# Performance work log

Measured on AMD Instinct MI355X. Metric: run time of the kernel, lower is better.

## Reference

```python
import jax, jax.numpy as jnp
import numpy as np

B, T, K = 1024, 1024, 48
START, STOP = 46, 47
NEG = -10000.0


def setup_inputs() -> dict:
    key = jax.random.key(0)
    k1, k2 = jax.random.split(key)
    feats = jax.random.normal(k1, (B, T, K), dtype=jnp.float32)
    transitions = jax.random.normal(k2, (K, K), dtype=jnp.float32)
    # CRF constraints exactly as in __init__: no transition into START, none out of STOP
    transitions = transitions.at[START, :].set(NEG).at[:, STOP].set(NEG)
    return {"feats": feats, "transitions": transitions}


def _viterbi_one(feats, transitions):
    # feats: [T, K]; transitions[next_tag, prev_tag]: [K, K]
    init = jnp.full((K,), NEG, dtype=feats.dtype).at[START].set(0.0)

    def step(forward_var, feat):
        # scores[next, prev] = forward_var[prev] + transitions[next, prev]
        scores = forward_var[None, :] + transitions
        bptr = jnp.argmax(scores, axis=1)                 # [K] best prev per next
        new_fv = jnp.max(scores, axis=1) + feat           # [K]
        return new_fv, bptr

    forward_var, bptrs = jax.lax.scan(step, init, feats)  # bptrs: [T, K]
    terminal = forward_var + transitions[STOP]
    best = jnp.argmax(terminal)
    path_score = terminal[best]

    # backtrack: carry = tag at time t, emit it, move to bptrs[t][tag]
    def back(tag, bp):
        return bp[tag], tag

    _, best_path = jax.lax.scan(back, best, bptrs, reverse=True)  # [T] in time order
    return path_score, best_path


def reference(feats, transitions):
    # vmap the (faithful, per-sequence) Viterbi decode over the batch
    scores, paths = jax.vmap(_viterbi_one, in_axes=(0, None))(feats, transitions)
    return scores, paths
```

## Files before the change

kernel.cpp:

```cpp
#include <hip/hip_runtime.h>
#include <float.h>


#define BB 1024
#define TT 1024
#define KK 48
#define CC 16
#define LL 64
#define NEGV -10000.0f

__device__ __forceinline__ float rdlane(float v, int l) {
  return __int_as_float(__builtin_amdgcn_readlane(__float_as_int(v), l));
}
__device__ __forceinline__ float max3f(float a, float b, float c) {
  return fmaxf(fmaxf(a, b), c);
}


#define FSTEP(T_, FEAT_)                                                   \
  {                                                                        \
    float fvs[KK];                                                         \
    _Pragma("unroll") for (int p = 0; p < KK; ++p) {                       \
      fvs[p] = rdlane(fv, p);                                              \
    }                                                                      \
    float s_[KK];                                                          \
    _Pragma("unroll") for (int p = 0; p < KK; ++p) {                       \
      s_[p] = fvs[p] + tr[p];                                              \
    }                                                                      \
    float part[16];                                                        \
    _Pragma("unroll") for (int g = 0; g < 16; ++g) {                       \
      part[g] = max3f(s_[3 * g], s_[3 * g + 1], s_[3 * g + 2]);            \
    }                                                                      \
    float q0 = max3f(part[0], part[1], part[2]);                           \
    float q1 = max3f(part[3], part[4], part[5]);                           \
    float q2 = max3f(part[6], part[7], part[8]);                           \
    float q3 = max3f(part[9], part[10], part[11]);                         \
    float q4 = max3f(part[12], part[13], part[14]);                        \
    float m_ = fmaxf(max3f(q0, q1, q2), max3f(q3, q4, part[15]));          \
    mp[(size_t)(T_)*KK] = m_;                                              \
    fv = m_ + (FEAT_);                                                     \
  }

__global__ __launch_bounds__(64, 1) void viterbi_fwd_mx(
    const float* __restrict__ feats, const float* __restrict__ trans,
    float* __restrict__ scores, float* __restrict__ mx,
    int* __restrict__ bestArr) {
  const int lane = threadIdx.x;
  const int b = blockIdx.x;
  const int rl = (lane < KK) ? lane : (KK - 1);

  float tr[KK];
#pragma unroll
  for (int j = 0; j < 12; ++j) {
    float4 t4 = *(const float4*)(trans + rl * KK + 4 * j);
    tr[4 * j + 0] = t4.x; tr[4 * j + 1] = t4.y;
    tr[4 * j + 2] = t4.z; tr[4 * j + 3] = t4.w;
  }
#pragma unroll
  for (int j = 0; j < KK; ++j) asm volatile("" : "+v"(tr[j]));
  const float tstop = trans[(KK - 1) * KK + rl];

  const float* fp = feats + (size_t)b * TT * KK + rl;
  float* mp = mx + (size_t)b * TT * KK + rl;

  float fv = (lane == 46) ? 0.0f : NEGV;

  float fA[8], fB[8];
#pragma unroll
  for (int k = 0; k < 8; ++k) fA[k] = fp[(size_t)k * KK];

  for (int t0 = 0; t0 < TT; t0 += 16) {
#pragma unroll
    for (int k = 0; k < 8; ++k)
      fB[k] = fp[(size_t)((t0 + 8 + k) & (TT - 1)) * KK];
#pragma unroll
    for (int u = 0; u < 8; ++u) FSTEP(t0 + u, fA[u]);
#pragma unroll
    for (int k = 0; k < 8; ++k)
      fA[k] = fp[(size_t)((t0 + 16 + k) & (TT - 1)) * KK];
#pragma unroll
    for (int u = 0; u < 8; ++u) FSTEP(t0 + 8 + u, fB[u]);
  }

  float v = (lane < KK) ? (fv + tstop) : -FLT_MAX;
  int idx = lane;
#pragma unroll
  for (int off = 32; off >= 1; off >>= 1) {
    float ov = __shfl_xor(v, off);
    int oi = __shfl_xor(idx, off);
    bool take = (ov > v) || (ov == v && oi < idx);
    v = take ? ov : v;
    idx = take ? oi : idx;
  }
  if (lane == 0) { scores[b] = v; bestArr[b] = idx; }
}

__global__ __launch_bounds__(64, 1) void viterbi_bwd_mx(
    const float* __restrict__ feats, const float* __restrict__ trans,
    const float* __restrict__ mx, const int* __restrict__ bestArr,
    float* __restrict__ path) {
  __shared__ float tl[KK * KK];
  const int lane = threadIdx.x;
  const int b = blockIdx.x;
  const int rl = (lane < KK) ? lane : (KK - 1);
  for (int i = lane; i < KK * KK; i += 64) tl[i] = trans[i];
  __syncthreads();

  const float* fp = feats + (size_t)b * TT * KK + rl;
  const float* mp = mx + (size_t)b * TT * KK + rl;
  int tag = bestArr[b];

  float topA = mp[(size_t)(TT - 1) * KK];
  float MA[8], FE[8], MB[8], FB2[8];
#pragma unroll
  for (int u = 0; u < 8; ++u) {
    MA[u] = mp[(size_t)(TT - 2 - u) * KK];
    FE[u] = fp[(size_t)(TT - 2 - u) * KK];
  }

  int myv = 0;
  for (int jb = TT - 1; jb >= 15; jb -= 16) {
#pragma unroll
    for (int u = 0; u < 8; ++u) {
      int r = jb - 9 - u; int rc = r < 0 ? 0 : r;
      MB[u] = mp[(size_t)rc * KK];
      FB2[u] = fp[(size_t)rc * KK];
    }
#pragma unroll
    for (int u = 0; u < 8; ++u) {
      const int j = jb - u;
      if (lane == (j & 63)) myv = tag;
      if ((j & 63) == 0) path[(size_t)b * TT + j + lane] = (float)myv;
      float Tg = (u == 0) ? topA : MA[u - 1];
      float target = rdlane(Tg, tag);
      float s = (MA[u] + FE[u]) + tl[tag * KK + rl];
      unsigned long long bal = __ballot(s == target);
      tag = (int)__builtin_ctzll(bal);
    }
    float topB = MA[7];
#pragma unroll
    for (int u = 0; u < 8; ++u) {
      int r = jb - 17 - u; int rc = r < 0 ? 0 : r;
      MA[u] = mp[(size_t)rc * KK];
      FE[u] = fp[(size_t)rc * KK];
    }
#pragma unroll
    for (int u = 0; u < 8; ++u) {
      const int j = jb - 8 - u;
      if (lane == (j & 63)) myv = tag;
      if ((j & 63) == 0) path[(size_t)b * TT + j + lane] = (float)myv;
      float Tg = (u == 0) ? topB : MB[u - 1];
      float target = rdlane(Tg, tag);
      float s = (MB[u] + FB2[u]) + tl[tag * KK + rl];
      unsigned long long bal = __ballot(s == target);
      tag = (int)__builtin_ctzll(bal);
    }
    topA = MB[7];
  }
}


__global__ __launch_bounds__(64, 1) void viterbi_fwd_f(
    const float* __restrict__ feats, const float* __restrict__ trans,
    float* __restrict__ scores, unsigned char* __restrict__ bptr,
    int* __restrict__ bestArr) {
  __shared__ __align__(16) float fvbuf[64];
  const int lane = threadIdx.x;
  const int b = blockIdx.x;
  const int rl = (lane < KK) ? lane : (KK - 1);

  float tr[KK];
#pragma unroll
  for (int j = 0; j < 12; ++j) {
    float4 t4 = *(const float4*)(trans + rl * KK + 4 * j);
    tr[4 * j + 0] = t4.x; tr[4 * j + 1] = t4.y;
    tr[4 * j + 2] = t4.z; tr[4 * j + 3] = t4.w;
  }
  const float tstop = trans[(KK - 1) * KK + rl];

  if (lane < KK) fvbuf[lane] = (lane == 46) ? 0.0f : NEGV;
  __builtin_amdgcn_wave_barrier();

  const float* fp = feats + (size_t)b * TT * KK + rl;
  unsigned char* bp = bptr + (size_t)b * TT * KK + lane;

  float fbuf[4];
#pragma unroll
  for (int k = 0; k < 4; ++k) fbuf[k] = fp[(size_t)k * KK];

  float fv = NEGV;
  for (int t0 = 0; t0 < TT; t0 += 4) {
#pragma unroll
    for (int u = 0; u < 4; ++u) {
      const int t = t0 + u;
      float fvr[KK];
#pragma unroll
      for (int j = 0; j < 12; ++j) {
        float4 v4 = *(const float4*)(&fvbuf[4 * j]);
        fvr[4 * j + 0] = v4.x; fvr[4 * j + 1] = v4.y;
        fvr[4 * j + 2] = v4.z; fvr[4 * j + 3] = v4.w;
      }
      __builtin_amdgcn_wave_barrier();

      float bs0 = fvr[0] + tr[0], bs1 = fvr[12] + tr[12];
      float bs2 = fvr[24] + tr[24], bs3 = fvr[36] + tr[36];
      int bi0 = 0, bi1 = 12, bi2 = 24, bi3 = 36;
#pragma unroll
      for (int p = 1; p < 12; ++p) {
        float s0 = fvr[p] + tr[p];
        float s1 = fvr[12 + p] + tr[12 + p];
        float s2 = fvr[24 + p] + tr[24 + p];
        float s3 = fvr[36 + p] + tr[36 + p];
        if (s0 > bs0) { bs0 = s0; bi0 = p; }
        if (s1 > bs1) { bs1 = s1; bi1 = 12 + p; }
        if (s2 > bs2) { bs2 = s2; bi2 = 24 + p; }
        if (s3 > bs3) { bs3 = s3; bi3 = 36 + p; }
      }
      bool c1 = bs1 > bs0;
      float m01 = c1 ? bs1 : bs0; int i01 = c1 ? bi1 : bi0;
      bool c3 = bs3 > bs2;
      float m23 = c3 ? bs3 : bs2; int i23 = c3 ? bi3 : bi2;
      bool cf = m23 > m01;
      float m = cf ? m23 : m01; int bpi = cf ? i23 : i01;

      float nfv = m + fbuf[u];
      int tpre = t + 4; if (tpre >= TT) tpre = 0;
      fbuf[u] = fp[(size_t)tpre * KK];

      if (lane < KK) {
        bp[(size_t)t * KK] = (unsigned char)bpi;
        fvbuf[lane] = nfv;
        fv = nfv;
      }
      __builtin_amdgcn_wave_barrier();
    }
  }

  float v = (lane < KK) ? (fv + tstop) : -FLT_MAX;
  int idx = lane;
#pragma unroll
  for (int off = 32; off >= 1; off >>= 1) {
    float ov = __shfl_xor(v, off);
    int oi = __shfl_xor(idx, off);
    bool take = (ov > v) || (ov == v && oi < idx);
    v = take ? ov : v;
    idx = take ? oi : idx;
  }
  if (lane == 0) { scores[b] = v; bestArr[b] = idx; }
}

__global__ __launch_bounds__(256) void bwd_map(
    const unsigned char* __restrict__ bptr, unsigned char* __restrict__ cmap) {
  const int lane = threadIdx.x & 63;
  const int wg = blockIdx.x * 4 + (threadIdx.x >> 6);
  const int b = wg >> 4;
  const int c = wg & (CC - 1);
  const int rl = (lane < KK) ? lane : (KK - 1);
  const unsigned char* bp = bptr + ((size_t)b * TT + (size_t)c * LL) * KK + rl;

  int x = rl;
  const int CH = 16;
  int cur[CH], nxt[CH];
#pragma unroll
  for (int j = 0; j < CH; ++j) cur[j] = bp[(size_t)(LL - CH + j) * KK];
  for (int tb = LL - CH; tb >= 0; tb -= CH) {
    if (tb >= CH) {
#pragma unroll
      for (int j = 0; j < CH; ++j) nxt[j] = bp[(size_t)(tb - CH + j) * KK];
    }
#pragma unroll
    for (int j = CH - 1; j >= 0; --j) x = __shfl(cur[j], x);
    if (tb >= CH) {
#pragma unroll
      for (int j = 0; j < CH; ++j) cur[j] = nxt[j];
    }
  }
  if (lane < KK) cmap[(size_t)wg * KK + lane] = (unsigned char)x;
}

__global__ __launch_bounds__(256) void bwd_entry(
    const unsigned char* __restrict__ cmap, const int* __restrict__ bestArr,
    int* __restrict__ entry) {
  const int lane = threadIdx.x & 63;
  const int b = blockIdx.x * 4 + (threadIdx.x >> 6);
  const int rl = (lane < KK) ? lane : (KK - 1);

  int rows[CC];
#pragma unroll
  for (int c = 0; c < CC; ++c) rows[c] = cmap[((size_t)b * CC + c) * KK + rl];

  int tag = bestArr[b];
  int ev = 0;
#pragma unroll
  for (int c = CC - 1; c >= 0; --c) {
    if (lane == c) ev = tag;
    tag = __shfl(rows[c], tag);
  }
  if (lane < CC) entry[b * CC + lane] = ev;
}

__global__ __launch_bounds__(256) void bwd_emit(
    const unsigned char* __restrict__ bptr, const int* __restrict__ entry,
    float* __restrict__ path) {
  const int lane = threadIdx.x & 63;
  const int wg = blockIdx.x * 4 + (threadIdx.x >> 6);
  const int b = wg >> 4;
  const int c = wg & (CC - 1);
  const int rl = (lane < KK) ? lane : (KK - 1);
  const unsigned char* bp = bptr + ((size_t)b * TT + (size_t)c * LL) * KK + rl;

  int x = entry[b * CC + c];
  int myv = 0;
  const int CH = 16;
  int cur[CH], nxt[CH];
#pragma unroll
  for (int j = 0; j < CH; ++j) cur[j] = bp[(size_t)(LL - CH + j) * KK];
  for (int tb = LL - CH; tb >= 0; tb -= CH) {
    if (tb >= CH) {
#pragma unroll
      for (int j = 0; j < CH; ++j) nxt[j] = bp[(size_t)(tb - CH + j) * KK];
    }
#pragma unroll
    for (int j = CH - 1; j >= 0; --j) {
      if (lane == tb + j) myv = x;
      x = __shfl(cur[j], x);
    }
    if (tb >= CH) {
#pragma unroll
      for (int j = 0; j < CH; ++j) cur[j] = nxt[j];
    }
  }
  path[(size_t)b * TT + (size_t)c * LL + lane] = (float)myv;
}

extern "C" void kernel_launch(void* const* d_in, const int* in_sizes, int n_in,
                              void* d_out, int out_size, void* d_ws,
                              size_t ws_size, hipStream_t stream) {
  const float* feats = (const float*)d_in[0];
  const float* trans = (const float*)d_in[1];
  float* out = (float*)d_out;

  const size_t MX_BYTES = (size_t)BB * TT * KK * sizeof(float);
  if (ws_size >= MX_BYTES + 4096) {
    float* mx = (float*)d_ws;
    int* bestArr = (int*)((char*)d_ws + MX_BYTES);
    viterbi_fwd_mx<<<dim3(BB), dim3(64), 0, stream>>>(feats, trans, out, mx,
                                                      bestArr);
    viterbi_bwd_mx<<<dim3(BB), dim3(64), 0, stream>>>(feats, trans, mx,
                                                      bestArr, out + BB);
  } else {
    unsigned char* bptr = (unsigned char*)d_ws;
    char* p = (char*)d_ws + (size_t)BB * TT * KK;
    int* bestArr = (int*)p;
    p += BB * sizeof(int);
    unsigned char* cmap = (unsigned char*)p;
    p += (size_t)BB * CC * KK;
    int* entry = (int*)p;

    viterbi_fwd_f<<<dim3(BB), dim3(64), 0, stream>>>(feats, trans, out, bptr,
                                                     bestArr);
    bwd_map<<<dim3(BB * CC / 4), dim3(256), 0, stream>>>(bptr, cmap);
    bwd_entry<<<dim3(BB / 4), dim3(256), 0, stream>>>(cmap, bestArr, entry);
    bwd_emit<<<dim3(BB * CC / 4), dim3(256), 0, stream>>>(bptr, entry,
                                                          out + BB);
  }
}
```

Before: 532.2 us.

## Split forward Viterbi max over two wavefronts with LDS-shared forward vars

The forward kernel now uses 128 threads. Each wavefront handles 24 next-tags, and each half-wave reduces over 24 previous tags, combining the halves with a shuffle. The forward vector is exchanged through a double-buffered LDS array with a block barrier every timestep, replacing the 48 readlane broadcasts per step. This shortens each step's serial max chain and halves the per-lane transition registers, at the cost of a __syncthreads and LDS round trip on every one of the 1024 steps.

```diff
diff --git a/kernel.cpp b/kernel.cpp
--- a/kernel.cpp
+++ b/kernel.cpp
@@ -17,53 +17,71 @@
 }
 
 
-#define FSTEP(T_, FEAT_)                                                   \
+#define FSTEP2(T_, FEAT_, CUR_)                                            \
   {                                                                        \
-    float fvs[KK];                                                         \
-    _Pragma("unroll") for (int p = 0; p < KK; ++p) {                       \
-      fvs[p] = rdlane(fv, p);                                              \
+    float fvr[24];                                                         \
+    _Pragma("unroll") for (int j = 0; j < 6; ++j) {                        \
+      float4 v4 = *(const float4*)(&fvbuf[(CUR_)][hbase + 4 * j]);         \
+      fvr[4 * j + 0] = v4.x; fvr[4 * j + 1] = v4.y;                        \
+      fvr[4 * j + 2] = v4.z; fvr[4 * j + 3] = v4.w;                        \
     }                                                                      \
-    float s_[KK];                                                          \
-    _Pragma("unroll") for (int p = 0; p < KK; ++p) {                       \
-      s_[p] = fvs[p] + tr[p];                                              \
+    float s_[24];                                                          \
+    _Pragma("unroll") for (int p = 0; p < 24; ++p) {                       \
+      s_[p] = fvr[p] + tr[p];                                              \
     }                                                                      \
-    float part[16];                                                        \
-    _Pragma("unroll") for (int g = 0; g < 16; ++g) {                       \
+    float part[8];                                                         \
+    _Pragma("unroll") for (int g = 0; g < 8; ++g) {                        \
       part[g] = max3f(s_[3 * g], s_[3 * g + 1], s_[3 * g + 2]);            \
     }                                                                      \
     float q0 = max3f(part[0], part[1], part[2]);                           \
     float q1 = max3f(part[3], part[4], part[5]);                           \
-    float q2 = max3f(part[6], part[7], part[8]);                           \
-    float q3 = max3f(part[9], part[10], part[11]);                         \
-    float q4 = max3f(part[12], part[13], part[14]);                        \
-    float m_ = fmaxf(max3f(q0, q1, q2), max3f(q3, q4, part[15]));          \
-    mp[(size_t)(T_)*KK] = m_;                                              \
+    float q2 = fmaxf(part[6], part[7]);                                    \
+    float pm = max3f(q0, q1, q2);                                          \
+    float om = __shfl_xor(pm, 32);                                         \
+    float m_ = fmaxf(pm, om);                                              \
+    if (stLane) mp[(size_t)(T_)*KK] = m_;                                  \
     fv = m_ + (FEAT_);                                                     \
-  }
-
-__global__ __launch_bounds__(64, 1) void viterbi_fwd_mx(
+    if (wrLane) fvbuf[(CUR_) ^ 1][nxt] = fv;                               \
+    __syncthreads();                                                       \
+  }
+
+__global__ __launch_bounds__(128, 1) void viterbi_fwd_mx(
     const float* __restrict__ feats, const float* __restrict__ trans,
     float* __restrict__ scores, float* __restrict__ mx,
     int* __restrict__ bestArr) {
-  const int lane = threadIdx.x;
+  __shared__ __align__(16) float fvbuf[2][KK];
+  __shared__ float sc[2];
+  __shared__ int si[2];
+  const int tid = threadIdx.x;
+  const int w = tid >> 6;
+  const int lane = tid & 63;
+  const int li = lane & 31;
+  const int h = lane >> 5;
+  const int lic = (li < 24) ? li : 23;
+  const int nxt = 24 * w + lic;
   const int b = blockIdx.x;
-  const int rl = (lane < KK) ? lane : (KK - 1);
-
-  float tr[KK];
-#pragma unroll
-  for (int j = 0; j < 12; ++j) {
-    float4 t4 = *(const float4*)(trans + rl * KK + 4 * j);
+  const bool wrLane = (h == 0) && (li < 24);
+  const bool stLane = (h == 1) && (li < 24);
+  const int hbase = 24 * h;
+
+  float tr[24];
+#pragma unroll
+  for (int j = 0; j < 6; ++j) {
+    float4 t4 = *(const float4*)(trans + nxt * KK + 24 * h + 4 * j);
     tr[4 * j + 0] = t4.x; tr[4 * j + 1] = t4.y;
     tr[4 * j + 2] = t4.z; tr[4 * j + 3] = t4.w;
   }
 #pragma unroll
-  for (int j = 0; j < KK; ++j) asm volatile("" : "+v"(tr[j]));
-  const float tstop = trans[(KK - 1) * KK + rl];
-
-  const float* fp = feats + (size_t)b * TT * KK + rl;
-  float* mp = mx + (size_t)b * TT * KK + rl;
-
-  float fv = (lane == 46) ? 0.0f : NEGV;
+  for (int j = 0; j < 24; ++j) asm volatile("" : "+v"(tr[j]));
+  const float tstop = trans[(KK - 1) * KK + nxt];
+
+  const float* fp = feats + (size_t)b * TT * KK + nxt;
+  float* mp = mx + (size_t)b * TT * KK + nxt;
+
+  if (tid < KK) fvbuf[0][tid] = (tid == 46) ? 0.0f : NEGV;
+  __syncthreads();
+
+  float fv = NEGV;
 
   float fA[8], fB[8];
 #pragma unroll
@@ -74,16 +92,16 @@
     for (int k = 0; k < 8; ++k)
       fB[k] = fp[(size_t)((t0 + 8 + k) & (TT - 1)) * KK];
 #pragma unroll
-    for (int u = 0; u < 8; ++u) FSTEP(t0 + u, fA[u]);
+    for (int u = 0; u < 8; ++u) FSTEP2(t0 + u, fA[u], (u & 1));
 #pragma unroll
     for (int k = 0; k < 8; ++k)
       fA[k] = fp[(size_t)((t0 + 16 + k) & (TT - 1)) * KK];
 #pragma unroll
-    for (int u = 0; u < 8; ++u) FSTEP(t0 + 8 + u, fB[u]);
-  }
-
-  float v = (lane < KK) ? (fv + tstop) : -FLT_MAX;
-  int idx = lane;
+    for (int u = 0; u < 8; ++u) FSTEP2(t0 + 8 + u, fB[u], (u & 1));
+  }
+
+  float v = wrLane ? (fv + tstop) : -FLT_MAX;
+  int idx = nxt;
 #pragma unroll
   for (int off = 32; off >= 1; off >>= 1) {
     float ov = __shfl_xor(v, off);
@@ -92,7 +110,14 @@
     v = take ? ov : v;
     idx = take ? oi : idx;
   }
-  if (lane == 0) { scores[b] = v; bestArr[b] = idx; }
+  if (lane == 0) { sc[w] = v; si[w] = idx; }
+  __syncthreads();
+  if (tid == 0) {
+    float v0 = sc[0], v1 = sc[1];
+    bool take = v1 > v0;
+    scores[b] = take ? v1 : v0;
+    bestArr[b] = take ? si[1] : si[0];
+  }
 }
 
 __global__ __launch_bounds__(64, 1) void viterbi_bwd_mx(
@@ -344,8 +369,8 @@
   if (ws_size >= MX_BYTES + 4096) {
     float* mx = (float*)d_ws;
     int* bestArr = (int*)((char*)d_ws + MX_BYTES);
-    viterbi_fwd_mx<<<dim3(BB), dim3(64), 0, stream>>>(feats, trans, out, mx,
-                                                      bestArr);
+    viterbi_fwd_mx<<<dim3(BB), dim3(128), 0, stream>>>(feats, trans, out, mx,
+                                                       bestArr);
     viterbi_bwd_mx<<<dim3(BB), dim3(64), 0, stream>>>(feats, trans, mx,
                                                       bestArr, out + BB);
   } else {
```

Measured after the change: 516.2 us. -3.0%, faster.
